# Kernel tuning notes

Hardware: AMD Instinct MI355X
Metric: run time of the kernel (lower is better)

Reference implementation:

```python
import jax, jax.numpy as jnp
import numpy as np

BATCH, TIME, NUM_CLASSES = 128, 512, 1024
SAMPLE_OUT_SIZE = TIME          # input_length == sample_out_size == time
DUMMY_WORD = 2
EPS = 1e-8


def setup_inputs() -> dict:
    key = jax.random.key(0)
    # class probabilities (layer applies log(inputs + 1e-8) itself)
    inputs = jax.random.uniform(key, (BATCH, TIME, NUM_CLASSES), dtype=jnp.float32)
    return {"inputs": inputs}


def reference(inputs):
    """CTC greedy decode (merge_repeated=False) + sparse_to_dense(default=-1)
    + pad with dummy_word, sliced to sample_out_size. Returns [B, T] int32."""
    B, T, V = inputs.shape
    blank = V - 1  # TF CTC blank label = num_classes - 1

    logp = jnp.log(inputs + EPS)                       # faithful to layer
    ids = jnp.argmax(logp, axis=-1)                    # [B, T] greedy path

    nonblank = ids != blank                            # merge_repeated=False: only drop blanks
    counts = jnp.sum(nonblank, axis=1)                 # [B] decoded length per row
    max_len = jnp.max(counts)                          # dense_shape[1] of the SparseTensor

    # stable left-compaction of non-blank tokens (argsort is stable in jax)
    keys = jnp.where(nonblank, 0, 1).astype(jnp.int32)
    order = jnp.argsort(keys, axis=1)                  # [B, T]
    compacted = jnp.take_along_axis(ids, order, axis=1)  # [B, T]

    pos = jnp.arange(T)[None, :]                       # [1, T]
    # j <  counts[b]        -> decoded token
    # counts[b] <= j < L    -> -1   (sparse_to_dense default)
    # L <= j < T            -> dummy_word (concatenated dummy vector)
    out = jnp.where(
        pos < counts[:, None],
        compacted,
        jnp.where(pos < max_len, -1, DUMMY_WORD),
    ).astype(jnp.int32)
    return out
```

## Files before the change

### kernel.cpp

```cpp
#include <hip/hip_runtime.h>
#include <hip/hip_bf16.h>

#define BATCH 128
#define TIME 512
#define NUM_CLASSES 1024
#define BLANK (NUM_CLASSES - 1)
#define DUMMY_WORD 2

__global__ __launch_bounds__(256) void argmax_kernel(
    const float* __restrict__ in, int* __restrict__ ids) {
    int wid = blockIdx.x * 4 + (threadIdx.x >> 6);
    int lane = threadIdx.x & 63;
    const float4* p = (const float4*)(in + (size_t)wid * NUM_CLASSES);

    float best = -1e30f;
    int bidx = 0;
#pragma unroll
    for (int k = 0; k < 4; k++) {
        float4 v = p[lane + k * 64];
        int base = 4 * (lane + k * 64);
        if (v.x > best) { best = v.x; bidx = base; }
        if (v.y > best) { best = v.y; bidx = base + 1; }
        if (v.z > best) { best = v.z; bidx = base + 2; }
        if (v.w > best) { best = v.w; bidx = base + 3; }
    }
#pragma unroll
    for (int m = 32; m >= 1; m >>= 1) {
        float ov = __shfl_xor(best, m, 64);
        int   oi = __shfl_xor(bidx, m, 64);
        if (ov > best || (ov == best && oi < bidx)) { best = ov; bidx = oi; }
    }
    if (lane == 0) ids[wid] = bidx;
}

__global__ __launch_bounds__(64) void compact_kernel(
    int* __restrict__ ids, int* __restrict__ counts) {
    int b = blockIdx.x;
    int lane = threadIdx.x;
    int* row = ids + b * TIME;

    const int4* r4 = (const int4*)row;
    int4 a = r4[lane * 2];
    int4 c = r4[lane * 2 + 1];
    int vals[8] = {a.x, a.y, a.z, a.w, c.x, c.y, c.z, c.w};

    int cnt = 0;
#pragma unroll
    for (int j = 0; j < 8; j++) cnt += (vals[j] != BLANK);

    int incl = cnt;
#pragma unroll
    for (int off = 1; off < 64; off <<= 1) {
        int n = __shfl_up(incl, off, 64);
        if (lane >= off) incl += n;
    }
    int pos = incl - cnt;
#pragma unroll
    for (int j = 0; j < 8; j++) {
        if (vals[j] != BLANK) { row[pos] = vals[j]; pos++; }
    }
    if (lane == 63) counts[b] = incl;
}

__global__ __launch_bounds__(512) void finalize_kernel(
    const int* __restrict__ counts, int* __restrict__ out) {
    __shared__ int smem[BATCH];
    __shared__ int s_max;
    int b = blockIdx.x;
    int t = threadIdx.x;
    if (t < BATCH) smem[t] = counts[t];
    __syncthreads();
    if (t == 0) {
        int m = 0;
        for (int i = 0; i < BATCH; i++) m = max(m, smem[i]);
        s_max = m;
    }
    __syncthreads();
    int cnt = smem[b];
    if (t >= cnt) out[b * TIME + t] = (t < s_max) ? -1 : DUMMY_WORD;
}

extern "C" void kernel_launch(void* const* d_in, const int* in_sizes, int n_in,
                              void* d_out, int out_size, void* d_ws, size_t ws_size,
                              hipStream_t stream) {
    const float* in = (const float*)d_in[0];
    int* out = (int*)d_out;
    int* counts = (int*)d_ws;

    argmax_kernel<<<(BATCH * TIME) / 4, 256, 0, stream>>>(in, out);
    compact_kernel<<<BATCH, 64, 0, stream>>>(out, counts);
    finalize_kernel<<<BATCH, 512, 0, stream>>>(counts, out);
}
```

Baseline: 351.8 us.

## Fuse argmax, compaction and finalize into one cooperative persistent kernel

Replaces three kernel launches with a single cooperative launch of 1024 blocks, each wave handling 16 rows for argmax in a loop, with grid-wide syncs between the argmax, compaction and finalize phases. This removes two launch gaps and the tail of the small follow-up kernels. In exchange the argmax phase runs a fixed persistent grid rather than one wave per row, and it adds the cost of two grid barriers. It also relies on cooperative launch residency: 1024 blocks of 256 threads must all be resident. The initial best value also changes from -1e30 to -1, which is valid only because the inputs are non-negative.

Result: slower. 587.8 us (+67.1%).

```diff
diff --git a/kernel.cpp b/kernel.cpp
--- a/kernel.cpp
+++ b/kernel.cpp
@@ -1,5 +1,8 @@
 #include <hip/hip_runtime.h>
 #include <hip/hip_bf16.h>
+#include <hip/hip_cooperative_groups.h>
+
+namespace cg = cooperative_groups;
 
 #define BATCH 128
 #define TIME 512
@@ -7,77 +10,85 @@
 #define BLANK (NUM_CLASSES - 1)
 #define DUMMY_WORD 2
 
-__global__ __launch_bounds__(256) void argmax_kernel(
-    const float* __restrict__ in, int* __restrict__ ids) {
-    int wid = blockIdx.x * 4 + (threadIdx.x >> 6);
-    int lane = threadIdx.x & 63;
-    const float4* p = (const float4*)(in + (size_t)wid * NUM_CLASSES);
+#define NBLK 1024
+#define NTHR 256
+#define NWAVES (NBLK * (NTHR / 64))
+#define POS_PER_WAVE ((BATCH * TIME) / NWAVES)
 
-    float best = -1e30f;
-    int bidx = 0;
+__global__ __launch_bounds__(NTHR, 4) void ctc_fused_kernel(
+    const float* __restrict__ in, int* __restrict__ out, int* __restrict__ counts) {
+    cg::grid_group grid = cg::this_grid();
+    const int tid = threadIdx.x;
+    const int lane = tid & 63;
+    const int w = blockIdx.x * (NTHR / 64) + (tid >> 6);
+
+    for (int i = 0; i < POS_PER_WAVE; i++) {
+        int pos = w * POS_PER_WAVE + i;
+        const float4* p = (const float4*)(in + (size_t)pos * NUM_CLASSES);
+        float best = -1.0f;
+        int bidx = 0;
 #pragma unroll
-    for (int k = 0; k < 4; k++) {
-        float4 v = p[lane + k * 64];
-        int base = 4 * (lane + k * 64);
-        if (v.x > best) { best = v.x; bidx = base; }
-        if (v.y > best) { best = v.y; bidx = base + 1; }
-        if (v.z > best) { best = v.z; bidx = base + 2; }
-        if (v.w > best) { best = v.w; bidx = base + 3; }
+        for (int k = 0; k < 4; k++) {
+            float4 v = p[lane + k * 64];
+            int base = 4 * (lane + k * 64);
+            if (v.x > best) { best = v.x; bidx = base; }
+            if (v.y > best) { best = v.y; bidx = base + 1; }
+            if (v.z > best) { best = v.z; bidx = base + 2; }
+            if (v.w > best) { best = v.w; bidx = base + 3; }
+        }
+#pragma unroll
+        for (int m = 32; m >= 1; m >>= 1) {
+            float ov = __shfl_xor(best, m, 64);
+            int   oi = __shfl_xor(bidx, m, 64);
+            if (ov > best || (ov == best && oi < bidx)) { best = ov; bidx = oi; }
+        }
+        if (lane == 0) out[pos] = bidx;
     }
+
+    grid.sync();
+
+    if (blockIdx.x < BATCH && tid < 64) {
+        int b = blockIdx.x;
+        int* row = out + b * TIME;
+        const int4* r4 = (const int4*)row;
+        int4 a = r4[lane * 2];
+        int4 c = r4[lane * 2 + 1];
+        int vals[8] = {a.x, a.y, a.z, a.w, c.x, c.y, c.z, c.w};
+        int cnt = 0;
 #pragma unroll
-    for (int m = 32; m >= 1; m >>= 1) {
-        float ov = __shfl_xor(best, m, 64);
-        int   oi = __shfl_xor(bidx, m, 64);
-        if (ov > best || (ov == best && oi < bidx)) { best = ov; bidx = oi; }
+        for (int j = 0; j < 8; j++) cnt += (vals[j] != BLANK);
+        int incl = cnt;
+#pragma unroll
+        for (int off = 1; off < 64; off <<= 1) {
+            int n = __shfl_up(incl, off, 64);
+            if (lane >= off) incl += n;
+        }
+        int pos = incl - cnt;
+#pragma unroll
+        for (int j = 0; j < 8; j++)
+            if (vals[j] != BLANK) { row[pos] = vals[j]; pos++; }
+        if (lane == 63) counts[b] = incl;
     }
-    if (lane == 0) ids[wid] = bidx;
-}
 
-__global__ __launch_bounds__(64) void compact_kernel(
-    int* __restrict__ ids, int* __restrict__ counts) {
-    int b = blockIdx.x;
-    int lane = threadIdx.x;
-    int* row = ids + b * TIME;
+    grid.sync();
 
-    const int4* r4 = (const int4*)row;
-    int4 a = r4[lane * 2];
-    int4 c = r4[lane * 2 + 1];
-    int vals[8] = {a.x, a.y, a.z, a.w, c.x, c.y, c.z, c.w};
-
-    int cnt = 0;
-#pragma unroll
-    for (int j = 0; j < 8; j++) cnt += (vals[j] != BLANK);
-
-    int incl = cnt;
-#pragma unroll
-    for (int off = 1; off < 64; off <<= 1) {
-        int n = __shfl_up(incl, off, 64);
-        if (lane >= off) incl += n;
+    if (blockIdx.x < BATCH) {
+        __shared__ int scnt[BATCH];
+        __shared__ int smax;
+        if (tid < BATCH) scnt[tid] = counts[tid];
+        __syncthreads();
+        if (tid == 0) {
+            int m = 0;
+            for (int i = 0; i < BATCH; i++) m = max(m, scnt[i]);
+            smax = m;
+        }
+        __syncthreads();
+        int b = blockIdx.x;
+        int cnt = scnt[b];
+        int maxlen = smax;
+        for (int t = tid; t < TIME; t += NTHR)
+            if (t >= cnt) out[b * TIME + t] = (t < maxlen) ? -1 : DUMMY_WORD;
     }
-    int pos = incl - cnt;
-#pragma unroll
-    for (int j = 0; j < 8; j++) {
-        if (vals[j] != BLANK) { row[pos] = vals[j]; pos++; }
-    }
-    if (lane == 63) counts[b] = incl;
-}
-
-__global__ __launch_bounds__(512) void finalize_kernel(
-    const int* __restrict__ counts, int* __restrict__ out) {
-    __shared__ int smem[BATCH];
-    __shared__ int s_max;
-    int b = blockIdx.x;
-    int t = threadIdx.x;
-    if (t < BATCH) smem[t] = counts[t];
-    __syncthreads();
-    if (t == 0) {
-        int m = 0;
-        for (int i = 0; i < BATCH; i++) m = max(m, smem[i]);
-        s_max = m;
-    }
-    __syncthreads();
-    int cnt = smem[b];
-    if (t >= cnt) out[b * TIME + t] = (t < s_max) ? -1 : DUMMY_WORD;
 }
 
 extern "C" void kernel_launch(void* const* d_in, const int* in_sizes, int n_in,
@@ -87,7 +98,7 @@
     int* out = (int*)d_out;
     int* counts = (int*)d_ws;
 
-    argmax_kernel<<<(BATCH * TIME) / 4, 256, 0, stream>>>(in, out);
-    compact_kernel<<<BATCH, 64, 0, stream>>>(out, counts);
-    finalize_kernel<<<BATCH, 512, 0, stream>>>(counts, out);
+    void* args[] = {(void*)&in, (void*)&out, (void*)&counts};
+    hipLaunchCooperativeKernel((void*)ctc_fused_kernel, dim3(NBLK), dim3(NTHR),
+                               args, 0, stream);
 }
```
